# Performance work log

Hardware: AMD Instinct MI355X
Metric: run time of the kernel (lower is better)

The kernel has to match this reference:

```python
import jax, jax.numpy as jnp
import numpy as np

N_NODES = 50000
N_EDGES = 400000
N_GRAPHS = 500
N_FEAT = 4
EMB = 200
HID = 128


def setup_inputs() -> dict:
    key = jax.random.key(0)
    ks = jax.random.split(key, 16)
    x = jax.random.normal(ks[0], (N_NODES, N_FEAT), dtype=jnp.float32)
    edge_index = jax.random.randint(ks[1], (2, N_EDGES), 0, N_NODES, dtype=jnp.int64)
    x_scalar = jax.random.normal(ks[2], (N_GRAPHS, N_FEAT), dtype=jnp.float32)
    batch_index = jnp.sort(jax.random.randint(ks[3], (N_NODES,), 0, N_GRAPHS, dtype=jnp.int64))

    def lin(k, fan_in, fan_out):
        return jax.random.normal(k, (fan_in, fan_out), dtype=jnp.float32) / np.sqrt(fan_in)

    params = {
        'W0': lin(ks[4], N_FEAT, EMB), 'b0': jnp.zeros((EMB,), jnp.float32),
        'W1': lin(ks[5], EMB, EMB), 'b1': jnp.zeros((EMB,), jnp.float32),
        'W2': lin(ks[6], EMB, EMB), 'b2': jnp.zeros((EMB,), jnp.float32),
        'W3': lin(ks[7], EMB, EMB), 'b3': jnp.zeros((EMB,), jnp.float32),
        'Wl1': lin(ks[8], EMB + N_FEAT, HID),
        'bl1': jax.random.normal(ks[9], (HID,), jnp.float32) * 0.01,
        'Wl2': lin(ks[10], HID, 1),
        'bl2': jax.random.normal(ks[11], (1,), jnp.float32) * 0.01,
    }
    return dict(x=x, edge_index=edge_index, x_scalar=x_scalar, batch_index=batch_index, **params)


def _gcn_conv(h, W, b, src, dst, norm, num_nodes):
    # PyG GCNConv: h' = D^-1/2 (A+I) D^-1/2 (h W) + b, with precomputed edge norms
    m = (h @ W)[src] * norm[:, None]            # [E+N, out]
    out = jax.ops.segment_sum(m, dst, num_segments=num_nodes)
    return out + b


def reference(x, edge_index, x_scalar, batch_index,
              W0, b0, W1, b1, W2, b2, W3, b3, Wl1, bl1, Wl2, bl2):
    num_nodes = x.shape[0]
    loops = jnp.arange(num_nodes, dtype=edge_index.dtype)
    src = jnp.concatenate([edge_index[0], loops])  # self-loops appended
    dst = jnp.concatenate([edge_index[1], loops])
    deg = jax.ops.segment_sum(jnp.ones_like(dst, dtype=x.dtype), dst, num_segments=num_nodes)
    dinv = deg ** -0.5                              # deg >= 1 due to self-loops
    norm = dinv[src] * dinv[dst]

    h = jax.nn.leaky_relu(_gcn_conv(x, W0, b0, src, dst, norm, num_nodes), 0.01)
    h = jax.nn.leaky_relu(_gcn_conv(h, W1, b1, src, dst, norm, num_nodes), 0.01)
    h = jax.nn.leaky_relu(_gcn_conv(h, W2, b2, src, dst, norm, num_nodes), 0.01)
    h = jax.nn.leaky_relu(_gcn_conv(h, W3, b3, src, dst, norm, num_nodes), 0.01)

    # global mean pool per graph
    sums = jax.ops.segment_sum(h, batch_index, num_segments=N_GRAPHS)
    cnt = jax.ops.segment_sum(jnp.ones((num_nodes,), h.dtype), batch_index, num_segments=N_GRAPHS)
    pooled = sums / jnp.maximum(cnt, 1.0)[:, None]

    g = jnp.concatenate([pooled, x_scalar], axis=1)   # [G, EMB+4]
    g = jax.nn.leaky_relu(g @ Wl1 + bl1, 0.01)
    out = g @ Wl2 + bl2                                # [G, 1]
    return out
```

## Files before the change

kernel.cpp:

```cpp
#include <hip/hip_runtime.h>
#include <math.h>

#define LEAKY(v) ((v) > 0.0f ? (v) : 0.01f * (v))

typedef _Float16 v8h __attribute__((ext_vector_type(8)));
typedef float v4f __attribute__((ext_vector_type(4)));

__global__ void k_zero(int* __restrict__ cnt, int n) {
    int i = blockIdx.x * blockDim.x + threadIdx.x;
    if (i < n) cnt[i] = 0;
}

__global__ void k_zerof(float* __restrict__ p, int n) {
    int i = blockIdx.x * blockDim.x + threadIdx.x;
    if (i < n) p[i] = 0.0f;
}

__global__ void k_count(const int* __restrict__ ei, int* __restrict__ cnt, int E) {
    int e = blockIdx.x * blockDim.x + threadIdx.x;
    if (e < E) atomicAdd(&cnt[ei[E + e]], 1);
}

__global__ __launch_bounds__(256) void k_scan1(const int* __restrict__ cnt,
                                               int* __restrict__ rowptr,
                                               int* __restrict__ bsum, int n) {
    __shared__ int s[256];
    int t = threadIdx.x, i = blockIdx.x * 256 + t;
    int v = (i < n) ? cnt[i] : 0;
    s[t] = v;
    __syncthreads();
    for (int off = 1; off < 256; off <<= 1) {
        int u = (t >= off) ? s[t - off] : 0;
        __syncthreads();
        s[t] += u;
        __syncthreads();
    }
    if (i < n) rowptr[i] = s[t] - v;
    if (t == 255) bsum[blockIdx.x] = s[255];
}

__global__ __launch_bounds__(256) void k_scan2(int* __restrict__ bsum, int nb) {
    __shared__ int s[256];
    int t = threadIdx.x;
    int v = (t < nb) ? bsum[t] : 0;
    s[t] = v;
    __syncthreads();
    for (int off = 1; off < 256; off <<= 1) {
        int u = (t >= off) ? s[t - off] : 0;
        __syncthreads();
        s[t] += u;
        __syncthreads();
    }
    if (t < nb) bsum[t] = s[t] - v;
}

__global__ __launch_bounds__(256) void k_scan3(int* __restrict__ rowptr,
                                               const int* __restrict__ bsum,
                                               const int* __restrict__ cnt,
                                               float* __restrict__ dinv, int n) {
    int i = blockIdx.x * 256 + threadIdx.x;
    if (i < n) {
        rowptr[i] += bsum[blockIdx.x];
        dinv[i] = rsqrtf(1.0f + (float)cnt[i]);
    }
}

__global__ void k_fill(const int* __restrict__ ei, const float* __restrict__ dinv,
                       int* __restrict__ rowptr, int2* __restrict__ adj, int E) {
    int e = blockIdx.x * blockDim.x + threadIdx.x;
    if (e < E) {
        int s = ei[e], d = ei[E + e];
        int pos = atomicAdd(&rowptr[d], 1);
        adj[pos] = make_int2(s, __float_as_int(dinv[s] * dinv[d]));
    }
}

__global__ __launch_bounds__(256) void k_splitW3(const float* __restrict__ W1,
                                                 const float* __restrict__ W2,
                                                 const float* __restrict__ W3,
                                                 _Float16* __restrict__ th0, _Float16* __restrict__ tl0,
                                                 _Float16* __restrict__ th1, _Float16* __restrict__ tl1,
                                                 _Float16* __restrict__ th2, _Float16* __restrict__ tl2) {
    int layer = blockIdx.y;
    const float* W = (layer == 0) ? W1 : (layer == 1) ? W2 : W3;
    _Float16* Wth = (layer == 0) ? th0 : (layer == 1) ? th1 : th2;
    _Float16* Wtl = (layer == 0) ? tl0 : (layer == 1) ? tl1 : tl2;
    int idx = blockIdx.x * blockDim.x + threadIdx.x;
    if (idx >= 224 * 208) return;
    int k = idx / 208, n = idx - k * 208;
    float v = (k < 200 && n < 200) ? W[k * 200 + n] : 0.0f;
    _Float16 hi = (_Float16)v;
    _Float16 lo = (_Float16)(v - (float)hi);
    Wth[n * 224 + k] = hi;
    Wtl[n * 224 + k] = lo;
}

__global__ void k_gather4(const float* __restrict__ x, const float* __restrict__ dinv,
                          const int* __restrict__ rowptr, const int2* __restrict__ adj,
                          float* __restrict__ px, int n) {
    int v = blockIdx.x * blockDim.x + threadIdx.x;
    if (v >= n) return;
    float w0 = dinv[v]; w0 *= w0;
    float4 xv = ((const float4*)x)[v];
    float4 acc = make_float4(xv.x * w0, xv.y * w0, xv.z * w0, xv.w * w0);
    int lo = v ? rowptr[v - 1] : 0;
    int hi = rowptr[v];
    for (int j = lo; j < hi; ++j) {
        int2 cw = adj[j];
        int s = cw.x; float w = __int_as_float(cw.y);
        float4 sv = ((const float4*)x)[s];
        acc.x += sv.x * w; acc.y += sv.y * w; acc.z += sv.z * w; acc.w += sv.w * w;
    }
    ((float4*)px)[v] = acc;
}

__global__ __launch_bounds__(256, 4) void k_gemm200_mfma_l0(const float* __restrict__ px,
                                                            const float* __restrict__ W0,
                                                            const float* __restrict__ b0,
                                                            const _Float16* __restrict__ Wth,
                                                            const _Float16* __restrict__ Wtl,
                                                            _Float16* __restrict__ T, int M) {
    __shared__ _Float16 Wsh[208 * 32];
    __shared__ _Float16 Wsl[208 * 32];
    __shared__ float W0s[4][200];
    __shared__ float b0s[200];
    const int tid  = threadIdx.x;
    const int lane = tid & 63;
    const int wid  = tid >> 6;
    const int quad = lane >> 4;
    const int l16  = lane & 15;
    const int rowA = blockIdx.x * 64 + wid * 16 + l16;
    const int rowAc = min(rowA, M - 1);
    const float4 pxv = ((const float4*)px)[rowAc];

    for (int idx = tid; idx < 1000; idx += 256) {
        if (idx < 800) W0s[idx / 200][idx % 200] = W0[idx];
        else b0s[idx - 800] = b0[idx - 800];
    }
    __syncthreads();

    v4f acc[13];
#pragma unroll
    for (int t = 0; t < 13; ++t) acc[t] = 0.0f;

    for (int k0 = 0; k0 < 224; k0 += 32) {
        v8h ah, al;
        int kb = k0 + quad * 8;
        if (kb < 200) {
#pragma unroll
            for (int j = 0; j < 8; ++j) {
                int k = kb + j;
                float pv = pxv.x * W0s[0][k] + pxv.y * W0s[1][k]
                         + pxv.z * W0s[2][k] + pxv.w * W0s[3][k] + b0s[k];
                pv = LEAKY(pv);
                _Float16 h = (_Float16)pv;
                ah[j] = h;
                al[j] = (_Float16)(pv - (float)h);
            }
        } else {
#pragma unroll
            for (int j = 0; j < 8; ++j) { ah[j] = (_Float16)0.0f; al[j] = (_Float16)0.0f; }
        }
        __syncthreads();
        for (int idx = tid; idx < 832; idx += 256) {
            int nr = idx >> 2, part = idx & 3;
            *(uint4*)&Wsh[nr * 32 + part * 8] = *(const uint4*)&Wth[nr * 224 + k0 + part * 8];
            *(uint4*)&Wsl[nr * 32 + part * 8] = *(const uint4*)&Wtl[nr * 224 + k0 + part * 8];
        }
        __syncthreads();
#pragma unroll
        for (int t = 0; t < 13; ++t) {
            int nidx = (t * 16 + l16) * 32 + quad * 8;
            v8h wh = *(const v8h*)&Wsh[nidx];
            v8h wl = *(const v8h*)&Wsl[nidx];
            acc[t] = __builtin_amdgcn_mfma_f32_16x16x32_f16(ah, wh, acc[t], 0, 0, 0);
            acc[t] = __builtin_amdgcn_mfma_f32_16x16x32_f16(ah, wl, acc[t], 0, 0, 0);
            acc[t] = __builtin_amdgcn_mfma_f32_16x16x32_f16(al, wh, acc[t], 0, 0, 0);
        }
    }
    const int rb = blockIdx.x * 64 + wid * 16 + quad * 4;
#pragma unroll
    for (int t = 0; t < 13; ++t) {
        int c = t * 16 + l16;
        if (c < 200) {
#pragma unroll
            for (int e = 0; e < 4; ++e) {
                int r = rb + e;
                if (r < M) T[(size_t)r * 200 + c] = (_Float16)acc[t][e];
            }
        }
    }
}

__global__ __launch_bounds__(256, 4) void k_gemm200_mfma(const _Float16* __restrict__ P,
                                                         const float* __restrict__ bias,
                                                         const _Float16* __restrict__ Wth,
                                                         const _Float16* __restrict__ Wtl,
                                                         _Float16* __restrict__ T, int M) {
    __shared__ _Float16 Wsh[208 * 32];
    __shared__ _Float16 Wsl[208 * 32];
    const int tid  = threadIdx.x;
    const int lane = tid & 63;
    const int wid  = tid >> 6;
    const int quad = lane >> 4;
    const int l16  = lane & 15;
    const int rowA = blockIdx.x * 64 + wid * 16 + l16;
    const int rowAc = min(rowA, M - 1);
    const _Float16* Prow = P + (size_t)rowAc * 200;

    v4f acc[13];
#pragma unroll
    for (int t = 0; t < 13; ++t) acc[t] = 0.0f;

    for (int k0 = 0; k0 < 224; k0 += 32) {
        v8h ah, al;
        int kb = k0 + quad * 8;
        if (kb < 200) {
            v8h ph = *(const v8h*)(Prow + kb);
            float4 ba = *(const float4*)(bias + kb);
            float4 bb = *(const float4*)(bias + kb + 4);
            float bv[8] = {ba.x, ba.y, ba.z, ba.w, bb.x, bb.y, bb.z, bb.w};
#pragma unroll
            for (int j = 0; j < 8; ++j) {
                float av = (float)ph[j] + bv[j];
                av = LEAKY(av);
                _Float16 h = (_Float16)av;
                ah[j] = h;
                al[j] = (_Float16)(av - (float)h);
            }
        } else {
#pragma unroll
            for (int j = 0; j < 8; ++j) { ah[j] = (_Float16)0.0f; al[j] = (_Float16)0.0f; }
        }
        __syncthreads();
        for (int idx = tid; idx < 832; idx += 256) {
            int nr = idx >> 2, part = idx & 3;
            *(uint4*)&Wsh[nr * 32 + part * 8] = *(const uint4*)&Wth[nr * 224 + k0 + part * 8];
            *(uint4*)&Wsl[nr * 32 + part * 8] = *(const uint4*)&Wtl[nr * 224 + k0 + part * 8];
        }
        __syncthreads();
#pragma unroll
        for (int t = 0; t < 13; ++t) {
            int nidx = (t * 16 + l16) * 32 + quad * 8;
            v8h wh = *(const v8h*)&Wsh[nidx];
            v8h wl = *(const v8h*)&Wsl[nidx];
            acc[t] = __builtin_amdgcn_mfma_f32_16x16x32_f16(ah, wh, acc[t], 0, 0, 0);
            acc[t] = __builtin_amdgcn_mfma_f32_16x16x32_f16(ah, wl, acc[t], 0, 0, 0);
            acc[t] = __builtin_amdgcn_mfma_f32_16x16x32_f16(al, wh, acc[t], 0, 0, 0);
        }
    }
    const int rb = blockIdx.x * 64 + wid * 16 + quad * 4;
#pragma unroll
    for (int t = 0; t < 13; ++t) {
        int c = t * 16 + l16;
        if (c < 200) {
#pragma unroll
            for (int e = 0; e < 4; ++e) {
                int r = rb + e;
                if (r < M) T[(size_t)r * 200 + c] = (_Float16)acc[t][e];
            }
        }
    }
}

__global__ __launch_bounds__(256) void k_gather200h(const _Float16* __restrict__ t,
                                                    const float* __restrict__ dinv,
                                                    const int* __restrict__ rowptr,
                                                    const int2* __restrict__ adj,
                                                    _Float16* __restrict__ p, int n) {
    int gid = blockIdx.x * blockDim.x + threadIdx.x;
    if (gid >= n * 25) return;
    int v = gid / 25, c8 = gid - v * 25;
    const v8h* tp = (const v8h*)t;
    float w0 = dinv[v]; w0 *= w0;
    v8h tv = tp[v * 25 + c8];
    float a0[8], a1[8];
#pragma unroll
    for (int i = 0; i < 8; ++i) { a0[i] = (float)tv[i] * w0; a1[i] = 0.0f; }
    int lo = v ? rowptr[v - 1] : 0;
    int hi = rowptr[v];
    int j = lo;
    for (; j + 1 < hi; j += 2) {
        int2 e0 = adj[j], e1 = adj[j + 1];
        float wa = __int_as_float(e0.y), wb = __int_as_float(e1.y);
        v8h s0 = tp[e0.x * 25 + c8];
        v8h s1 = tp[e1.x * 25 + c8];
#pragma unroll
        for (int i = 0; i < 8; ++i) {
            a0[i] += (float)s0[i] * wa;
            a1[i] += (float)s1[i] * wb;
        }
    }
    if (j < hi) {
        int2 cw = adj[j];
        float w = __int_as_float(cw.y);
        v8h sv = tp[cw.x * 25 + c8];
#pragma unroll
        for (int i = 0; i < 8; ++i) a0[i] += (float)sv[i] * w;
    }
    v8h o;
#pragma unroll
    for (int i = 0; i < 8; ++i) o[i] = (_Float16)(a0[i] + a1[i]);
    ((v8h*)p)[v * 25 + c8] = o;
}

__global__ __launch_bounds__(256) void k_poolsum(const _Float16* __restrict__ p3,
                                                 const float* __restrict__ b3,
                                                 const int* __restrict__ batch, int n,
                                                 float* __restrict__ pooled) {
    int c = threadIdx.x;
    if (c >= 200) return;
    int base = blockIdx.x * 64;
    int end = min(base + 64, n);
    float bc = b3[c];
    int gprev = batch[base];
    float s = 0.0f;
    for (int i = base; i < end; ++i) {
        int g = batch[i];
        float v = (float)p3[(size_t)i * 200 + c] + bc;
        v = LEAKY(v);
        if (g != gprev) {
            atomicAdd(&pooled[gprev * 200 + c], s);
            s = 0.0f;
            gprev = g;
        }
        s += v;
    }
    atomicAdd(&pooled[gprev * 200 + c], s);
}

__global__ __launch_bounds__(128) void k_mlpfin(const float* __restrict__ pooled,
                                                const int* __restrict__ batch, int n_nodes,
                                                const float* __restrict__ xs,
                                                const float* __restrict__ Wl1,
                                                const float* __restrict__ bl1,
                                                const float* __restrict__ Wl2,
                                                const float* __restrict__ bl2,
                                                float* __restrict__ out) {
    __shared__ float grow[204];
    __shared__ float partial[2];
    __shared__ int sb[2];
    int g = blockIdx.x;
    int t = threadIdx.x;
    if (t == 0) {
        int lo = 0, hi = n_nodes;
        while (lo < hi) { int m = (lo + hi) >> 1; if (batch[m] < g) lo = m + 1; else hi = m; }
        sb[0] = lo;
        int lo2 = lo, hi2 = n_nodes;
        while (lo2 < hi2) { int m = (lo2 + hi2) >> 1; if (batch[m] < g + 1) lo2 = m + 1; else hi2 = m; }
        sb[1] = lo2;
    }
    __syncthreads();
    float inv = 1.0f / fmaxf((float)(sb[1] - sb[0]), 1.0f);
    for (int idx = t; idx < 200; idx += 128) grow[idx] = pooled[g * 200 + idx] * inv;
    if (t < 4) grow[200 + t] = xs[g * 4 + t];
    __syncthreads();
    float s = bl1[t];
    for (int k = 0; k < 204; ++k) s += grow[k] * Wl1[k * 128 + t];
    s = LEAKY(s);
    float hv = s * Wl2[t];
    for (int off = 32; off > 0; off >>= 1) hv += __shfl_down(hv, off, 64);
    if ((t & 63) == 0) partial[t >> 6] = hv;
    __syncthreads();
    if (t == 0) out[g] = partial[0] + partial[1] + bl2[0];
}

extern "C" void kernel_launch(void* const* d_in, const int* in_sizes, int n_in,
                              void* d_out, int out_size, void* d_ws, size_t ws_size,
                              hipStream_t stream) {
    const float* x    = (const float*)d_in[0];
    const int*   ei   = (const int*)d_in[1];
    const float* xs   = (const float*)d_in[2];
    const int*   batch= (const int*)d_in[3];
    const float* W0   = (const float*)d_in[4];
    const float* b0   = (const float*)d_in[5];
    const float* W1   = (const float*)d_in[6];
    const float* b1   = (const float*)d_in[7];
    const float* W2   = (const float*)d_in[8];
    const float* b2   = (const float*)d_in[9];
    const float* W3   = (const float*)d_in[10];
    const float* b3   = (const float*)d_in[11];
    const float* Wl1  = (const float*)d_in[12];
    const float* bl1  = (const float*)d_in[13];
    const float* Wl2  = (const float*)d_in[14];
    const float* bl2  = (const float*)d_in[15];
    float* out = (float*)d_out;

    const int N = in_sizes[0] / 4;
    const int E = in_sizes[1] / 2;
    const int G = in_sizes[2] / 4;

    char* ws = (char*)d_ws;
    size_t off = 0;
    auto alloc = [&](size_t bytes) { void* p = ws + off; off += (bytes + 255) & ~size_t(255); return p; };
    _Float16* bufA = (_Float16*)alloc((size_t)N * 200 * sizeof(_Float16));
    _Float16* bufB = (_Float16*)alloc((size_t)N * 200 * sizeof(_Float16));
    float* dinv   = (float*)alloc((size_t)N * sizeof(float));
    float* px     = (float*)alloc((size_t)N * 4 * sizeof(float));
    float* pooled = (float*)alloc((size_t)G * 200 * sizeof(float));
    int*   cnt    = (int*)alloc((size_t)N * sizeof(int));
    int*   rowptr = (int*)alloc(((size_t)N + 1) * sizeof(int));
    int*   bsum   = (int*)alloc(256 * sizeof(int));
    int2*  adj    = (int2*)alloc((size_t)E * sizeof(int2));
    _Float16* Wth[3]; _Float16* Wtl[3];
    for (int i = 0; i < 3; ++i) {
        Wth[i] = (_Float16*)alloc(208 * 224 * sizeof(_Float16));
        Wtl[i] = (_Float16*)alloc(208 * 224 * sizeof(_Float16));
    }

    const int B = 256;
    const int nblk = (N + 255) / 256;
    k_zero<<<(N + B - 1) / B, B, 0, stream>>>(cnt, N);
    k_count<<<(E + B - 1) / B, B, 0, stream>>>(ei, cnt, E);
    k_scan1<<<nblk, 256, 0, stream>>>(cnt, rowptr, bsum, N);
    k_scan2<<<1, 256, 0, stream>>>(bsum, nblk);
    k_scan3<<<nblk, 256, 0, stream>>>(rowptr, bsum, cnt, dinv, N);
    k_fill<<<(E + B - 1) / B, B, 0, stream>>>(ei, dinv, rowptr, adj, E);

    k_zerof<<<(G * 200 + B - 1) / B, B, 0, stream>>>(pooled, G * 200);

    dim3 sg((224 * 208 + B - 1) / B, 3);
    k_splitW3<<<sg, B, 0, stream>>>(W1, W2, W3, Wth[0], Wtl[0], Wth[1], Wtl[1], Wth[2], Wtl[2]);

    k_gather4<<<(N + B - 1) / B, B, 0, stream>>>(x, dinv, rowptr, adj, px, N);

    const int gblocks = (N * 25 + 255) / 256;

    k_gemm200_mfma_l0<<<(N + 63) / 64, 256, 0, stream>>>(px, W0, b0, Wth[0], Wtl[0], bufA, N);
    k_gather200h<<<gblocks, 256, 0, stream>>>(bufA, dinv, rowptr, adj, bufB, N);

    k_gemm200_mfma<<<(N + 63) / 64, 256, 0, stream>>>(bufB, b1, Wth[1], Wtl[1], bufA, N);
    k_gather200h<<<gblocks, 256, 0, stream>>>(bufA, dinv, rowptr, adj, bufB, N);
    k_gemm200_mfma<<<(N + 63) / 64, 256, 0, stream>>>(bufB, b2, Wth[2], Wtl[2], bufA, N);
    k_gather200h<<<gblocks, 256, 0, stream>>>(bufA, dinv, rowptr, adj, bufB, N);

    k_poolsum<<<(N + 63) / 64, 256, 0, stream>>>(bufB, b3, batch, N, pooled);
    k_mlpfin<<<G, 128, 0, stream>>>(pooled, batch, N, xs, Wl1, bl1, Wl2, bl2, out);
}
```

Measured before the change: 365.3 us.

## Fuse final gather with mean-pool, layer-0 gather into GEMM, zeroing into scan

Fuses the last neighbor aggregation with bias, activation and per-graph pooling, so the intermediate node features are no longer written and re-read. It also folds the 4-feature aggregation into the layer-0 GEMM prologue and moves pooled-buffer zeroing into the scan kernel, which removes three launches. In exchange, pooling now issues one float atomicAdd per node feature element into a small contended buffer instead of per-block segment reductions. Floating-point summation order also becomes nondeterministic at a finer grain.

```diff
diff --git a/kernel.cpp b/kernel.cpp
--- a/kernel.cpp
+++ b/kernel.cpp
@@ -9,11 +9,6 @@
 __global__ void k_zero(int* __restrict__ cnt, int n) {
     int i = blockIdx.x * blockDim.x + threadIdx.x;
     if (i < n) cnt[i] = 0;
-}
-
-__global__ void k_zerof(float* __restrict__ p, int n) {
-    int i = blockIdx.x * blockDim.x + threadIdx.x;
-    if (i < n) p[i] = 0.0f;
 }
 
 __global__ void k_count(const int* __restrict__ ei, int* __restrict__ cnt, int E) {
@@ -57,12 +52,14 @@
 __global__ __launch_bounds__(256) void k_scan3(int* __restrict__ rowptr,
                                                const int* __restrict__ bsum,
                                                const int* __restrict__ cnt,
-                                               float* __restrict__ dinv, int n) {
+                                               float* __restrict__ dinv, int n,
+                                               float* __restrict__ pooled, int npool) {
     int i = blockIdx.x * 256 + threadIdx.x;
     if (i < n) {
         rowptr[i] += bsum[blockIdx.x];
         dinv[i] = rsqrtf(1.0f + (float)cnt[i]);
     }
+    for (int j = i; j < npool; j += gridDim.x * 256) pooled[j] = 0.0f;
 }
 
 __global__ void k_fill(const int* __restrict__ ei, const float* __restrict__ dinv,
@@ -95,26 +92,10 @@
     Wtl[n * 224 + k] = lo;
 }
 
-__global__ void k_gather4(const float* __restrict__ x, const float* __restrict__ dinv,
-                          const int* __restrict__ rowptr, const int2* __restrict__ adj,
-                          float* __restrict__ px, int n) {
-    int v = blockIdx.x * blockDim.x + threadIdx.x;
-    if (v >= n) return;
-    float w0 = dinv[v]; w0 *= w0;
-    float4 xv = ((const float4*)x)[v];
-    float4 acc = make_float4(xv.x * w0, xv.y * w0, xv.z * w0, xv.w * w0);
-    int lo = v ? rowptr[v - 1] : 0;
-    int hi = rowptr[v];
-    for (int j = lo; j < hi; ++j) {
-        int2 cw = adj[j];
-        int s = cw.x; float w = __int_as_float(cw.y);
-        float4 sv = ((const float4*)x)[s];
-        acc.x += sv.x * w; acc.y += sv.y * w; acc.z += sv.z * w; acc.w += sv.w * w;
-    }
-    ((float4*)px)[v] = acc;
-}
-
-__global__ __launch_bounds__(256, 4) void k_gemm200_mfma_l0(const float* __restrict__ px,
+__global__ __launch_bounds__(256, 4) void k_gemm200_mfma_l0(const float* __restrict__ x,
+                                                            const float* __restrict__ dinv,
+                                                            const int* __restrict__ rowptr,
+                                                            const int2* __restrict__ adj,
                                                             const float* __restrict__ W0,
                                                             const float* __restrict__ b0,
                                                             const _Float16* __restrict__ Wth,
@@ -131,7 +112,20 @@
     const int l16  = lane & 15;
     const int rowA = blockIdx.x * 64 + wid * 16 + l16;
     const int rowAc = min(rowA, M - 1);
-    const float4 pxv = ((const float4*)px)[rowAc];
+
+    float w0n = dinv[rowAc]; w0n *= w0n;
+    float4 xv = ((const float4*)x)[rowAc];
+    float4 pxv = make_float4(xv.x * w0n, xv.y * w0n, xv.z * w0n, xv.w * w0n);
+    {
+        int lo = rowAc ? rowptr[rowAc - 1] : 0;
+        int hi = rowptr[rowAc];
+        for (int j = lo; j < hi; ++j) {
+            int2 cw = adj[j];
+            float w = __int_as_float(cw.y);
+            float4 sv = ((const float4*)x)[cw.x];
+            pxv.x += sv.x * w; pxv.y += sv.y * w; pxv.z += sv.z * w; pxv.w += sv.w * w;
+        }
+    }
 
     for (int idx = tid; idx < 1000; idx += 256) {
         if (idx < 800) W0s[idx / 200][idx % 200] = W0[idx];
@@ -304,29 +298,51 @@
     ((v8h*)p)[v * 25 + c8] = o;
 }
 
-__global__ __launch_bounds__(256) void k_poolsum(const _Float16* __restrict__ p3,
-                                                 const float* __restrict__ b3,
-                                                 const int* __restrict__ batch, int n,
-                                                 float* __restrict__ pooled) {
-    int c = threadIdx.x;
-    if (c >= 200) return;
-    int base = blockIdx.x * 64;
-    int end = min(base + 64, n);
-    float bc = b3[c];
-    int gprev = batch[base];
-    float s = 0.0f;
-    for (int i = base; i < end; ++i) {
-        int g = batch[i];
-        float v = (float)p3[(size_t)i * 200 + c] + bc;
-        v = LEAKY(v);
-        if (g != gprev) {
-            atomicAdd(&pooled[gprev * 200 + c], s);
-            s = 0.0f;
-            gprev = g;
-        }
-        s += v;
-    }
-    atomicAdd(&pooled[gprev * 200 + c], s);
+__global__ __launch_bounds__(256) void k_gatherpool(const _Float16* __restrict__ t,
+                                                    const float* __restrict__ dinv,
+                                                    const int* __restrict__ rowptr,
+                                                    const int2* __restrict__ adj,
+                                                    const int* __restrict__ batch,
+                                                    const float* __restrict__ b3,
+                                                    float* __restrict__ pooled, int n) {
+    int gid = blockIdx.x * blockDim.x + threadIdx.x;
+    if (gid >= n * 25) return;
+    int v = gid / 25, c8 = gid - v * 25;
+    const v8h* tp = (const v8h*)t;
+    float w0 = dinv[v]; w0 *= w0;
+    v8h tv = tp[v * 25 + c8];
+    float a0[8], a1[8];
+#pragma unroll
+    for (int i = 0; i < 8; ++i) { a0[i] = (float)tv[i] * w0; a1[i] = 0.0f; }
+    int lo = v ? rowptr[v - 1] : 0;
+    int hi = rowptr[v];
+    int j = lo;
+    for (; j + 1 < hi; j += 2) {
+        int2 e0 = adj[j], e1 = adj[j + 1];
+        float wa = __int_as_float(e0.y), wb = __int_as_float(e1.y);
+        v8h s0 = tp[e0.x * 25 + c8];
+        v8h s1 = tp[e1.x * 25 + c8];
+#pragma unroll
+        for (int i = 0; i < 8; ++i) {
+            a0[i] += (float)s0[i] * wa;
+            a1[i] += (float)s1[i] * wb;
+        }
+    }
+    if (j < hi) {
+        int2 cw = adj[j];
+        float w = __int_as_float(cw.y);
+        v8h sv = tp[cw.x * 25 + c8];
+#pragma unroll
+        for (int i = 0; i < 8; ++i) a0[i] += (float)sv[i] * w;
+    }
+    int g = batch[v];
+    float* pg = &pooled[g * 200 + c8 * 8];
+#pragma unroll
+    for (int i = 0; i < 8; ++i) {
+        float val = a0[i] + a1[i] + b3[c8 * 8 + i];
+        val = LEAKY(val);
+        atomicAdd(pg + i, val);
+    }
 }
 
 __global__ __launch_bounds__(128) void k_mlpfin(const float* __restrict__ pooled,
@@ -396,7 +412,6 @@
     _Float16* bufA = (_Float16*)alloc((size_t)N * 200 * sizeof(_Float16));
     _Float16* bufB = (_Float16*)alloc((size_t)N * 200 * sizeof(_Float16));
     float* dinv   = (float*)alloc((size_t)N * sizeof(float));
-    float* px     = (float*)alloc((size_t)N * 4 * sizeof(float));
     float* pooled = (float*)alloc((size_t)G * 200 * sizeof(float));
     int*   cnt    = (int*)alloc((size_t)N * sizeof(int));
     int*   rowptr = (int*)alloc(((size_t)N + 1) * sizeof(int));
@@ -414,26 +429,22 @@
     k_count<<<(E + B - 1) / B, B, 0, stream>>>(ei, cnt, E);
     k_scan1<<<nblk, 256, 0, stream>>>(cnt, rowptr, bsum, N);
     k_scan2<<<1, 256, 0, stream>>>(bsum, nblk);
-    k_scan3<<<nblk, 256, 0, stream>>>(rowptr, bsum, cnt, dinv, N);
+    k_scan3<<<nblk, 256, 0, stream>>>(rowptr, bsum, cnt, dinv, N, pooled, G * 200);
     k_fill<<<(E + B - 1) / B, B, 0, stream>>>(ei, dinv, rowptr, adj, E);
-
-    k_zerof<<<(G * 200 + B - 1) / B, B, 0, stream>>>(pooled, G * 200);
 
     dim3 sg((224 * 208 + B - 1) / B, 3);
     k_splitW3<<<sg, B, 0, stream>>>(W1, W2, W3, Wth[0], Wtl[0], Wth[1], Wtl[1], Wth[2], Wtl[2]);
 
-    k_gather4<<<(N + B - 1) / B, B, 0, stream>>>(x, dinv, rowptr, adj, px, N);
-
     const int gblocks = (N * 25 + 255) / 256;
 
-    k_gemm200_mfma_l0<<<(N + 63) / 64, 256, 0, stream>>>(px, W0, b0, Wth[0], Wtl[0], bufA, N);
+    k_gemm200_mfma_l0<<<(N + 63) / 64, 256, 0, stream>>>(x, dinv, rowptr, adj, W0, b0,
+                                                         Wth[0], Wtl[0], bufA, N);
     k_gather200h<<<gblocks, 256, 0, stream>>>(bufA, dinv, rowptr, adj, bufB, N);
 
     k_gemm200_mfma<<<(N + 63) / 64, 256, 0, stream>>>(bufB, b1, Wth[1], Wtl[1], bufA, N);
     k_gather200h<<<gblocks, 256, 0, stream>>>(bufA, dinv, rowptr, adj, bufB, N);
     k_gemm200_mfma<<<(N + 63) / 64, 256, 0, stream>>>(bufB, b2, Wth[2], Wtl[2], bufA, N);
-    k_gather200h<<<gblocks, 256, 0, stream>>>(bufA, dinv, rowptr, adj, bufB, N);
-
-    k_poolsum<<<(N + 63) / 64, 256, 0, stream>>>(bufB, b3, batch, N, pooled);
+
+    k_gatherpool<<<gblocks, 256, 0, stream>>>(bufA, dinv, rowptr, adj, batch, b3, pooled, N);
     k_mlpfin<<<G, 128, 0, stream>>>(pooled, batch, N, xs, Wl1, bl1, Wl2, bl2, out);
 }
```

New measurement: 702.8 us. 92.4% more time.
